# Kernel optimization log

Hardware: AMD Instinct MI355X
Metric: run time of the kernel (lower is better)

The kernel has to match this reference:

```python
import jax, jax.numpy as jnp
import numpy as np

VOCAB, D_MODEL, N_STATE, H_HEADS, LAYERS = 64, 512, 32, 16, 4
EXPAND = 2
D_INNER = EXPAND * D_MODEL          # 1024
P_HEAD = D_INNER // H_HEADS         # 64
CONV_DIM = D_INNER + 2 * N_STATE    # x, B, C share the depthwise conv
K_CONV = 4
D_IN_PROJ = 2 * D_INNER + 2 * N_STATE + H_HEADS  # z, x, B, C, dt
BATCH, SEQ = 4, 1024
EPS = 1e-5


def rmsnorm(x, w):
    return x * jax.lax.rsqrt(jnp.mean(x * x, axis=-1, keepdims=True) + EPS) * w


def silu(x):
    return x * jax.nn.sigmoid(x)


def causal_depthwise_conv(x, w, b):
    # x: [B,L,C], w: [C,K], b: [C]; causal (left) padding, depthwise groups
    xt = jnp.transpose(x, (0, 2, 1))  # [B,C,L]
    out = jax.lax.conv_general_dilated(xt, w[:, None, :], (1,), [(K_CONV - 1, 0)], feature_group_count=w.shape[0])
    return jnp.transpose(out, (0, 2, 1)) + b


def ssd(xh, dt, A, Bm, Cm, Dp):
    # Mamba2 SSD recurrence. xh [B,L,H,P], dt [B,L,H], A [H], Bm/Cm [B,L,N], Dp [H]
    dA = jnp.exp(dt * A)              # decay per (batch, step, head)
    dtx = dt[..., None] * xh          # [B,L,H,P]

    def step(h, inp):
        dA_t, dtx_t, B_t, C_t = inp
        # h: [B,H,P,N]
        h = dA_t[:, :, None, None] * h + dtx_t[..., None] * B_t[:, None, None, :]
        y = jnp.einsum('bhpn,bn->bhp', h, C_t)
        return h, y

    h0 = jnp.zeros((xh.shape[0], H_HEADS, P_HEAD, N_STATE), xh.dtype)
    _, ys = jax.lax.scan(step, h0, (jnp.moveaxis(dA, 1, 0), jnp.moveaxis(dtx, 1, 0), jnp.moveaxis(Bm, 1, 0), jnp.moveaxis(Cm, 1, 0)))
    return jnp.moveaxis(ys, 0, 1) + xh * Dp[None, None, :, None]


def mamba_block(x, norm_w, W_in, b_in, conv_w, conv_b, dt_bias, A_log, Dp, gnorm_w, W_out, b_out):
    res = x
    u = rmsnorm(x, norm_w)
    zxbcdt = u @ W_in + b_in                                # [B,L,D_IN_PROJ]
    z = zxbcdt[..., :D_INNER]
    xBC = zxbcdt[..., D_INNER:D_INNER + CONV_DIM]
    dt = zxbcdt[..., D_INNER + CONV_DIM:]                   # [B,L,H]
    xBC = silu(causal_depthwise_conv(xBC, conv_w, conv_b))
    xc = xBC[..., :D_INNER]
    Bm = xBC[..., D_INNER:D_INNER + N_STATE]
    Cm = xBC[..., D_INNER + N_STATE:]
    dt = jax.nn.softplus(dt + dt_bias)
    xh = xc.reshape(xc.shape[0], xc.shape[1], H_HEADS, P_HEAD)
    y = ssd(xh, dt, -jnp.exp(A_log), Bm, Cm, Dp)
    y = y.reshape(y.shape[0], y.shape[1], D_INNER)
    y = rmsnorm(y * silu(z), gnorm_w)                       # gated RMSNorm
    return res + y @ W_out + b_out


def forward(input_tokens, emb, norm_w, W_in, b_in, conv_w, conv_b, dt_bias, A_log, D_param, gnorm_w, W_out, b_out, head_w, head_b):
    h = emb[input_tokens]
    for i in range(LAYERS):
        h = mamba_block(h, norm_w[i], W_in[i], b_in[i], conv_w[i], conv_b[i], dt_bias[i], A_log[i], D_param[i], gnorm_w[i], W_out[i], b_out[i])
    return h @ head_w + head_b


def setup_inputs() -> dict:
    key = jax.random.key(0)
    ks = jax.random.split(key, 8)
    s = 0.02
    return {
        'input_tokens': jax.random.randint(ks[0], (BATCH, SEQ), 0, VOCAB),
        'emb': jax.random.normal(ks[1], (VOCAB, D_MODEL), jnp.float32) * s,
        'norm_w': jnp.ones((LAYERS, D_MODEL), jnp.float32),
        'W_in': jax.random.normal(ks[2], (LAYERS, D_MODEL, D_IN_PROJ), jnp.float32) * s,
        'b_in': jnp.zeros((LAYERS, D_IN_PROJ), jnp.float32),
        'conv_w': jax.random.normal(ks[3], (LAYERS, CONV_DIM, K_CONV), jnp.float32) * 0.1,
        'conv_b': jnp.zeros((LAYERS, CONV_DIM), jnp.float32),
        'dt_bias': jnp.tile(jnp.log(jnp.expm1(jnp.linspace(0.001, 0.1, H_HEADS, dtype=jnp.float32))), (LAYERS, 1)),
        'A_log': jnp.tile(jnp.log(jnp.arange(1, H_HEADS + 1, dtype=jnp.float32)), (LAYERS, 1)),
        'D_param': jnp.ones((LAYERS, H_HEADS), jnp.float32),
        'gnorm_w': jnp.ones((LAYERS, D_INNER), jnp.float32),
        'W_out': jax.random.normal(ks[4], (LAYERS, D_INNER, D_MODEL), jnp.float32) * s,
        'b_out': jnp.zeros((LAYERS, D_MODEL), jnp.float32),
        'head_w': jax.random.normal(ks[5], (D_MODEL, VOCAB), jnp.float32) * s,
        'head_b': jnp.zeros((VOCAB,), jnp.float32),
    }


def reference(input_tokens, emb, norm_w, W_in, b_in, conv_w, conv_b, dt_bias, A_log, D_param, gnorm_w, W_out, b_out, head_w, head_b):
    return forward(input_tokens, emb, norm_w, W_in, b_in, conv_w, conv_b, dt_bias, A_log, D_param, gnorm_w, W_out, b_out, head_w, head_b)
```

## Files before the change

### kernel.cpp

```cpp
#include <hip/hip_runtime.h>
#include <hip/hip_bf16.h>

#define VOCAB     64
#define D_MODEL   512
#define N_STATE   32
#define H_HEADS   16
#define LAYERS    4
#define D_INNER   1024
#define P_HEAD    64
#define CONV_DIM  1088
#define K_CONV    4
#define D_IN_PROJ 2128
#define NPAD_IN   2176
#define NPAD_HEAD 64
#define BATCH     4
#define SEQ       1024
#define NTOK      (BATCH*SEQ)
#define EPS       1e-5f
#define CL        64
#define NC        (SEQ/CL)
#define PSTR      80

typedef __bf16 bf16x8 __attribute__((ext_vector_type(8)));
typedef float  f32x4  __attribute__((ext_vector_type(4)));

__device__ __forceinline__ float sigmoidf_(float x) { return 1.f / (1.f + __expf(-x)); }
__device__ __forceinline__ float softplusf_(float x) { return (x > 20.f) ? x : log1pf(__expf(x)); }

__device__ __forceinline__ void gload_lds16(const void* g, void* l) {
  __builtin_amdgcn_global_load_lds((const __attribute__((address_space(1))) void*)g,
                                   (__attribute__((address_space(3))) void*)l,
                                   16, 0, 0);
}

__device__ __forceinline__ int xcd_lin() {
  return (blockIdx.x & 7) * ((int)gridDim.x >> 3) + ((int)blockIdx.x >> 3);
}

__global__ __launch_bounds__(256) void embed_kernel(
    const int* __restrict__ tok, const float* __restrict__ emb,
    float* __restrict__ h, __bf16* __restrict__ hbf) {
  int wv = threadIdx.x >> 6, lane = threadIdx.x & 63;
  int tokid = blockIdx.x * 4 + wv;
  const float* er = emb + (size_t)tok[tokid] * D_MODEL;
  f32x4 v0 = *(const f32x4*)(er + lane * 8);
  f32x4 v1 = *(const f32x4*)(er + lane * 8 + 4);
  float* hr = h + (size_t)tokid * D_MODEL;
  *(f32x4*)(hr + lane * 8) = v0;
  *(f32x4*)(hr + lane * 8 + 4) = v1;
  bf16x8 o8;
  #pragma unroll
  for (int k = 0; k < 4; k++) { o8[k] = (__bf16)v0[k]; o8[4 + k] = (__bf16)v1[k]; }
  *(bf16x8*)(hbf + (size_t)tokid * D_MODEL + lane * 8) = o8;
}

__global__ __launch_bounds__(256) void transpose_all_kernel(
    const float* __restrict__ W_in, const float* __restrict__ W_out,
    const float* __restrict__ head_w,
    const float* __restrict__ norm_w, const float* __restrict__ gnorm_w,
    __bf16* __restrict__ WtIn, __bf16* __restrict__ WtOut, __bf16* __restrict__ WtHead) {
  int b = blockIdx.x;
  const float* W; const float* fold; __bf16* Wt; int K, N, Npad, bx, by;
  if (b < 4352) {
    int z = b / 1088, r = b % 1088;
    bx = r % 68; by = r / 68;
    W = W_in + (size_t)z * D_MODEL * D_IN_PROJ;
    fold = norm_w + (size_t)z * D_MODEL;
    Wt = WtIn + (size_t)z * NPAD_IN * D_MODEL;
    K = D_MODEL; N = D_IN_PROJ; Npad = NPAD_IN;
  } else if (b < 6400) {
    int r = b - 4352; int z = r / 512; r %= 512;
    bx = r % 16; by = r / 16;
    W = W_out + (size_t)z * D_INNER * D_MODEL;
    fold = gnorm_w + (size_t)z * D_INNER;
    Wt = WtOut + (size_t)z * D_MODEL * D_INNER;
    K = D_INNER; N = D_MODEL; Npad = D_MODEL;
  } else {
    int r = b - 6400;
    bx = r % 2; by = r / 2;
    W = head_w; fold = nullptr; Wt = WtHead;
    K = D_MODEL; N = VOCAB; Npad = NPAD_HEAD;
  }
  __shared__ float T[32][33];
  int n0 = bx * 32, k0 = by * 32;
  int tx = threadIdx.x & 31, ty = threadIdx.x >> 5;
  #pragma unroll
  for (int i = 0; i < 4; i++) {
    int n = n0 + tx;
    T[ty + i * 8][tx] = (n < N) ? W[(size_t)(k0 + ty + i * 8) * N + n] : 0.f;
  }
  __syncthreads();
  float fs = fold ? fold[k0 + tx] : 1.f;
  #pragma unroll
  for (int i = 0; i < 4; i++)
    Wt[(size_t)(n0 + ty + i * 8) * K + k0 + tx] = (__bf16)(T[tx][ty + i * 8] * fs);
}

#define TK 64
__global__ __launch_bounds__(256) void gemm64_kernel(
    const __bf16* __restrict__ A, const __bf16* __restrict__ Bt,
    const float* __restrict__ bias, const float* __restrict__ res,
    float* __restrict__ C, __bf16* __restrict__ Cbf,
    float inv_norm_dim, int nbx, int K, int N, int ldc) {
  __shared__ __bf16 As[2][64 * TK];
  __shared__ __bf16 Bs[2][64 * TK];
  int tid = threadIdx.x;
  int lane = tid & 63, wave = tid >> 6;
  int wm = wave >> 1, wn = wave & 1;
  int q = lane >> 4, l16 = lane & 15;
  int lin = xcd_lin();
  int bx = lin % nbx, by = lin / nbx;
  size_t row0 = (size_t)by * 64;
  int col0 = bx * 64;
  const __bf16* Ab = A + row0 * K;
  const __bf16* Bb = Bt + (size_t)col0 * K;

  auto stage = [&](int buf, int kk) {
    #pragma unroll
    for (int r = 0; r < 2; r++) {
      int lin2 = r * 256 + tid;
      size_t goff = (size_t)(lin2 >> 3) * K + kk + (lin2 & 7) * 8;
      gload_lds16(Ab + goff, &As[buf][lin2 * 8]);
      gload_lds16(Bb + goff, &Bs[buf][lin2 * 8]);
    }
  };

  f32x4 acc[2][2];
  #pragma unroll
  for (int i = 0; i < 2; i++)
    #pragma unroll
    for (int j = 0; j < 2; j++) acc[i][j] = (f32x4){0.f, 0.f, 0.f, 0.f};
  float ssqa[2] = {0.f, 0.f};

  stage(0, 0);
  int cur = 0;
  for (int k0 = 0; k0 < K; k0 += TK) {
    if (k0 + TK < K) {
      stage(cur ^ 1, k0 + TK);
      asm volatile("s_waitcnt vmcnt(4)" ::: "memory");
    } else {
      asm volatile("s_waitcnt vmcnt(0)" ::: "memory");
    }
    __builtin_amdgcn_s_barrier();
    #pragma unroll
    for (int ks = 0; ks < 2; ks++) {
      bf16x8 af[2], bfv[2];
      #pragma unroll
      for (int i = 0; i < 2; i++) {
        af[i] = *(const bf16x8*)(&As[cur][(wm * 32 + i * 16 + l16) * TK + ks * 32 + q * 8]);
        #pragma unroll
        for (int k = 0; k < 8; k++) { float v = (float)af[i][k]; ssqa[i] += v * v; }
      }
      #pragma unroll
      for (int j = 0; j < 2; j++)
        bfv[j] = *(const bf16x8*)(&Bs[cur][(wn * 32 + j * 16 + l16) * TK + ks * 32 + q * 8]);
      #pragma unroll
      for (int i = 0; i < 2; i++)
        #pragma unroll
        for (int j = 0; j < 2; j++)
          acc[i][j] = __builtin_amdgcn_mfma_f32_16x16x32_bf16(af[i], bfv[j], acc[i][j], 0, 0, 0);
    }
    __builtin_amdgcn_s_barrier();
    cur ^= 1;
  }

  #pragma unroll
  for (int i = 0; i < 2; i++) {
    ssqa[i] += __shfl_xor(ssqa[i], 16);
    ssqa[i] += __shfl_xor(ssqa[i], 32);
  }
  #pragma unroll
  for (int i = 0; i < 2; i++) {
    #pragma unroll
    for (int rr = 0; rr < 4; rr++) {
      size_t mrow = row0 + wm * 32 + i * 16 + q * 4 + rr;
      float sq = __shfl(ssqa[i], q * 4 + rr);
      float sc = (inv_norm_dim > 0.f) ? rsqrtf(sq * inv_norm_dim + EPS) : 1.f;
      #pragma unroll
      for (int j = 0; j < 2; j++) {
        int col = col0 + wn * 32 + j * 16 + l16;
        if (col < N) {
          size_t off = mrow * (size_t)ldc + col;
          float v = acc[i][j][rr] * sc + (bias ? bias[col] : 0.f);
          if (res) v += res[off];
          if (C)   C[off] = v;
          if (Cbf) Cbf[off] = (__bf16)v;
        }
      }
    }
  }
}

__global__ __launch_bounds__(256) void gemm_in_kernel(
    const __bf16* __restrict__ A, const __bf16* __restrict__ Bt,
    const float* __restrict__ bias, __bf16* __restrict__ Cbf,
    int nbx, int K, int N, int ldc) {
  __shared__ __bf16 As[2][64 * TK];
  __shared__ __bf16 Bs[2][128 * TK];
  int tid = threadIdx.x;
  int lane = tid & 63, wave = tid >> 6;
  int wm = wave >> 1, wn = wave & 1;
  int q = lane >> 4, l16 = lane & 15;
  int lin = xcd_lin();
  int bx = lin % nbx, by = lin / nbx;
  size_t row0 = (size_t)by * 64;
  int col0 = bx * 128;
  const __bf16* Ab = A + row0 * K;
  const __bf16* Bb = Bt + (size_t)col0 * K;

  auto stage = [&](int buf, int kk) {
    #pragma unroll
    for (int r = 0; r < 2; r++) {
      int lin2 = r * 256 + tid;
      gload_lds16(Ab + (size_t)(lin2 >> 3) * K + kk + (lin2 & 7) * 8, &As[buf][lin2 * 8]);
    }
    #pragma unroll
    for (int r = 0; r < 4; r++) {
      int lin2 = r * 256 + tid;
      gload_lds16(Bb + (size_t)(lin2 >> 3) * K + kk + (lin2 & 7) * 8, &Bs[buf][lin2 * 8]);
    }
  };

  f32x4 acc[2][4];
  #pragma unroll
  for (int i = 0; i < 2; i++)
    #pragma unroll
    for (int j = 0; j < 4; j++) acc[i][j] = (f32x4){0.f, 0.f, 0.f, 0.f};
  float ssqa[2] = {0.f, 0.f};

  stage(0, 0);
  int cur = 0;
  for (int k0 = 0; k0 < K; k0 += TK) {
    if (k0 + TK < K) {
      stage(cur ^ 1, k0 + TK);
      asm volatile("s_waitcnt vmcnt(6)" ::: "memory");
    } else {
      asm volatile("s_waitcnt vmcnt(0)" ::: "memory");
    }
    __builtin_amdgcn_s_barrier();
    #pragma unroll
    for (int ks = 0; ks < 2; ks++) {
      bf16x8 af[2], bfv[4];
      #pragma unroll
      for (int i = 0; i < 2; i++) {
        af[i] = *(const bf16x8*)(&As[cur][(wm * 32 + i * 16 + l16) * TK + ks * 32 + q * 8]);
        #pragma unroll
        for (int k = 0; k < 8; k++) { float v = (float)af[i][k]; ssqa[i] += v * v; }
      }
      #pragma unroll
      for (int j = 0; j < 4; j++)
        bfv[j] = *(const bf16x8*)(&Bs[cur][(wn * 64 + j * 16 + l16) * TK + ks * 32 + q * 8]);
      #pragma unroll
      for (int i = 0; i < 2; i++)
        #pragma unroll
        for (int j = 0; j < 4; j++)
          acc[i][j] = __builtin_amdgcn_mfma_f32_16x16x32_bf16(af[i], bfv[j], acc[i][j], 0, 0, 0);
    }
    __builtin_amdgcn_s_barrier();
    cur ^= 1;
  }

  #pragma unroll
  for (int i = 0; i < 2; i++) {
    ssqa[i] += __shfl_xor(ssqa[i], 16);
    ssqa[i] += __shfl_xor(ssqa[i], 32);
  }
  __bf16* Cs = (__bf16*)Bs;
  const int CST = 136;
  float bvj[4];
  #pragma unroll
  for (int j = 0; j < 4; j++) {
    int colj = col0 + wn * 64 + j * 16 + l16;
    bvj[j] = (colj < N) ? bias[colj] : 0.f;
  }
  #pragma unroll
  for (int i = 0; i < 2; i++) {
    #pragma unroll
    for (int rr = 0; rr < 4; rr++) {
      int rloc = wm * 32 + i * 16 + q * 4 + rr;
      float sq = __shfl(ssqa[i], q * 4 + rr);
      float sc = rsqrtf(sq * (1.f / D_MODEL) + EPS);
      #pragma unroll
      for (int j = 0; j < 4; j++)
        Cs[rloc * CST + wn * 64 + j * 16 + l16] = (__bf16)(acc[i][j][rr] * sc + bvj[j]);
    }
  }
  __syncthreads();
  #pragma unroll
  for (int s = 0; s < 2; s++) {
    int idx = s * 256 + tid;
    int row = idx >> 3, c0 = (idx & 7) * 16;
    if (col0 + c0 < N) {
      bf16x8 v0 = *(const bf16x8*)(&Cs[row * CST + c0]);
      bf16x8 v1 = *(const bf16x8*)(&Cs[row * CST + c0 + 8]);
      __bf16* dst = Cbf + (row0 + row) * (size_t)ldc + col0 + c0;
      *(bf16x8*)dst = v0;
      *(bf16x8*)(dst + 8) = v1;
    }
  }
}

__device__ __forceinline__ void wave0_dt_cumsum(
    const __bf16* __restrict__ zxbf, const float* __restrict__ dt_bias,
    int b, int h, int t0, int tid, float* ldt, float* lcs, float* __restrict__ dtcsg) {
  if (tid < 64) {
    float dv = (float)zxbf[((size_t)(b * SEQ + t0 + tid)) * D_IN_PROJ + 2 * D_INNER + 2 * N_STATE + h]
               + dt_bias[h];
    float dtv = softplusf_(dv);
    float cs = dtv;
    #pragma unroll
    for (int off = 1; off < 64; off <<= 1) {
      float o = __shfl_up(cs, off);
      if (tid >= off) cs += o;
    }
    ldt[tid] = dtv;
    lcs[tid] = cs;
    dtcsg[tid] = dtv;
    dtcsg[64 + tid] = cs;
  }
}

__global__ __launch_bounds__(256) void ssd_local_kernel(
    const __bf16* __restrict__ zxbf, const float* __restrict__ conv_w,
    const float* __restrict__ conv_b, const float* __restrict__ dt_bias,
    const float* __restrict__ A_log,
    float* __restrict__ Slocal, float* __restrict__ dAprod,
    __bf16* __restrict__ convx, __bf16* __restrict__ convbc, float* __restrict__ dtcs) {
  int blk = xcd_lin();
  int c = blk % NC;
  int h = (blk / NC) % H_HEADS;
  int b = blk / (NC * H_HEADS);
  int tid = threadIdx.x;
  int lane = tid & 63, wave = tid >> 6;
  int q = lane >> 4, l16 = lane & 15;
  int t0 = c * CL;
  float A = -__expf(A_log[h]);
  __shared__ __bf16 rawbuf[2 * 68 * 64];
  __shared__ __bf16 lxT[64][PSTR];
  __shared__ __bf16 lBTw[32][PSTR];
  __shared__ float ldt[64], lcs[64];
  __bf16* rawx = rawbuf;
  __bf16* rawBC = rawbuf + 68 * 64;
  for (int i = tid; i < 68 * 8; i += 256) {
    int r = i >> 3, c0 = (i & 7) * 8;
    int gr = t0 - 3 + r;
    bf16x8 vx, vbc;
    #pragma unroll
    for (int k = 0; k < 8; k++) { vx[k] = (__bf16)0.f; vbc[k] = (__bf16)0.f; }
    if (gr >= 0) {
      const __bf16* rowp = zxbf + ((size_t)(b * SEQ + gr)) * D_IN_PROJ;
      vx  = *(const bf16x8*)(rowp + D_INNER + h * 64 + c0);
      vbc = *(const bf16x8*)(rowp + 2 * D_INNER + c0);
    }
    *(bf16x8*)(rawx + r * 64 + c0)  = vx;
    *(bf16x8*)(rawBC + r * 64 + c0) = vbc;
  }
  wave0_dt_cumsum(zxbf, dt_bias, b, h, t0, tid, ldt, lcs, dtcs + (size_t)blk * 128);
  __syncthreads();
  float cs63 = lcs[63];
  __bf16* xg  = convx  + (size_t)blk * 4096;
  __bf16* bcg = convbc + (size_t)blk * 4096;
  {
    int p = tid & 63;
    const float* w = conv_w + (h * 64 + p) * K_CONV;
    float w0 = w[0], w1 = w[1], w2 = w[2], w3 = w[3];
    float cb = conv_b[h * 64 + p];
    for (int i = tid; i < CL * 64; i += 256) {
      int t = i >> 6;
      float a = cb + w0 * (float)rawx[t * 64 + p] + w1 * (float)rawx[(t + 1) * 64 + p]
                   + w2 * (float)rawx[(t + 2) * 64 + p] + w3 * (float)rawx[(t + 3) * 64 + p];
      lxT[p][t] = (__bf16)(a * sigmoidf_(a));
    }
  }
  {
    int col = tid & 63;
    const float* w = conv_w + (D_INNER + col) * K_CONV;
    float w0 = w[0], w1 = w[1], w2 = w[2], w3 = w[3];
    float cb = conv_b[D_INNER + col];
    for (int i = tid; i < CL * 64; i += 256) {
      int t = i >> 6;
      float a = cb + w0 * (float)rawBC[t * 64 + col] + w1 * (float)rawBC[(t + 1) * 64 + col]
                   + w2 * (float)rawBC[(t + 2) * 64 + col] + w3 * (float)rawBC[(t + 3) * 64 + col];
      float v = a * sigmoidf_(a);
      if (col < 32) {
        bcg[t * 32 + col] = (__bf16)v;
        float wt = ldt[t] * __expf(A * (cs63 - lcs[t]));
        lBTw[col][t] = (__bf16)(v * wt);
      } else {
        bcg[2048 + t * 32 + (col - 32)] = (__bf16)v;
      }
    }
  }
  __syncthreads();
  #pragma unroll
  for (int s = 0; s < 2; s++) {
    int idx = s * 256 + tid;
    int row = idx >> 3, c0 = (idx & 7) * 8;
    *(bf16x8*)(xg + row * 64 + c0) = *(const bf16x8*)(&lxT[row][c0]);
  }
  f32x4 acc0 = (f32x4){0.f,0.f,0.f,0.f}, acc1 = (f32x4){0.f,0.f,0.f,0.f};
  #pragma unroll
  for (int kb = 0; kb < 2; kb++) {
    bf16x8 af = *(const bf16x8*)(&lxT[wave * 16 + l16][kb * 32 + q * 8]);
    bf16x8 b0 = *(const bf16x8*)(&lBTw[l16][kb * 32 + q * 8]);
    bf16x8 b1 = *(const bf16x8*)(&lBTw[l16 + 16][kb * 32 + q * 8]);
    acc0 = __builtin_amdgcn_mfma_f32_16x16x32_bf16(af, b0, acc0, 0, 0, 0);
    acc1 = __builtin_amdgcn_mfma_f32_16x16x32_bf16(af, b1, acc1, 0, 0, 0);
  }
  float* sT = (float*)rawbuf;
  #pragma unroll
  for (int rr = 0; rr < 4; rr++) {
    int p = wave * 16 + q * 4 + rr;
    sT[p * 36 + l16]      = acc0[rr];
    sT[p * 36 + l16 + 16] = acc1[rr];
  }
  {
    int row = tid >> 2, c0 = (tid & 3) * 8;
    f32x4 a = *(const f32x4*)(sT + row * 36 + c0);
    f32x4 b2 = *(const f32x4*)(sT + row * 36 + c0 + 4);
    float* dstp = Slocal + (size_t)blk * 2048 + row * 32 + c0;
    *(f32x4*)dstp = a;
    *(f32x4*)(dstp + 4) = b2;
  }
  if (tid == 0) dAprod[blk] = __expf(A * cs63);
}

__global__ __launch_bounds__(256) void ssd_out_kernel(
    const __bf16* __restrict__ zxbf, const float* __restrict__ A_log,
    const float* __restrict__ Dp,
    const float* __restrict__ Slocal, const float* __restrict__ dAprod,
    const __bf16* __restrict__ convx, const __bf16* __restrict__ convbc,
    const float* __restrict__ dtcs, __bf16* __restrict__ gout) {
  int blk = xcd_lin();
  int c = blk % NC;
  int h = (blk / NC) % H_HEADS;
  int b = blk / (NC * H_HEADS);
  int tid = threadIdx.x;
  int lane = tid & 63, wave = tid >> 6;
  int q = lane >> 4, l16 = lane & 15;
  int t0 = c * CL;
  float A = -__expf(A_log[h]);
  float D = Dp[h];
  __shared__ __bf16 lxT[64][PSTR];
  __shared__ __bf16 pPbuf[64 * PSTR];
  __shared__ __bf16 lB[64][32];
  __shared__ __bf16 lC[64][32];
  __shared__ __bf16 lS[64][32];
  __shared__ float ldt[64], lcs[64];
  __shared__ float pr[NC];
  const __bf16* xg  = convx  + (size_t)blk * 4096;
  const __bf16* bcg = convbc + (size_t)blk * 4096;
  #pragma unroll
  for (int s = 0; s < 2; s++) {
    int idx = s * 256 + tid;
    int row = idx >> 3, c0 = (idx & 7) * 8;
    *(bf16x8*)(&lxT[row][c0]) = *(const bf16x8*)(xg + row * 64 + c0);
  }
  {
    int row = tid >> 2, c0 = (tid & 3) * 8;
    *(bf16x8*)(&lB[row][c0]) = *(const bf16x8*)(bcg + row * 32 + c0);
    *(bf16x8*)(&lC[row][c0]) = *(const bf16x8*)(bcg + 2048 + row * 32 + c0);
  }
  if (tid < 64) {
    const float* dg = dtcs + (size_t)blk * 128;
    ldt[tid] = dg[tid];
    lcs[tid] = dg[64 + tid];
  }
  if (tid < NC) pr[tid] = dAprod[(blk - c) + tid];
  __syncthreads();
  {
    int p = tid >> 2, n0 = (tid & 3) * 8;
    const float* sl = Slocal + (size_t)(blk - c) * 2048 + p * 32 + n0;
    float st[8] = {};
    for (int j = 0; j < c; j++) {
      f32x4 a = *(const f32x4*)(sl + (size_t)j * 2048);
      f32x4 bq = *(const f32x4*)(sl + (size_t)j * 2048 + 4);
      float prj = pr[j];
      #pragma unroll
      for (int k = 0; k < 4; k++) { st[k] = prj * st[k] + a[k]; st[4 + k] = prj * st[4 + k] + bq[k]; }
    }
    #pragma unroll
    for (int k = 0; k < 8; k++) lS[p][n0 + k] = (__bf16)st[k];
  }
  __syncthreads();
  bf16x8 afC = *(const bf16x8*)(&lC[wave * 16 + l16][q * 8]);
  f32x4 accG[4], accI[4], accY[4];
  #pragma unroll
  for (int j = 0; j < 4; j++) {
    accG[j] = (f32x4){0.f,0.f,0.f,0.f};
    accI[j] = (f32x4){0.f,0.f,0.f,0.f};
    accY[j] = (f32x4){0.f,0.f,0.f,0.f};
  }
  #pragma unroll
  for (int j = 0; j < 4; j++) {
    bf16x8 bf = *(const bf16x8*)(&lB[l16 + 16 * j][q * 8]);
    accG[j] = __builtin_amdgcn_mfma_f32_16x16x32_bf16(afC, bf, accG[j], 0, 0, 0);
  }
  #pragma unroll
  for (int j = 0; j < 4; j++) {
    bf16x8 bf = *(const bf16x8*)(&lS[l16 + 16 * j][q * 8]);
    accI[j] = __builtin_amdgcn_mfma_f32_16x16x32_bf16(afC, bf, accI[j], 0, 0, 0);
  }
  __bf16* pP = pPbuf + wave * 16 * PSTR;
  #pragma unroll
  for (int j = 0; j < 4; j++) {
    int s = l16 + 16 * j;
    float css = lcs[s], dts = ldt[s];
    #pragma unroll
    for (int rr = 0; rr < 4; rr++) {
      int tl = q * 4 + rr;
      int t = wave * 16 + tl;
      float val = accG[j][rr] * __expf(A * (lcs[t] - css)) * dts;
      if (s == t) val += D;
      if (s > t) val = 0.f;
      pP[tl * PSTR + s] = (__bf16)val;
    }
  }
  #pragma unroll
  for (int kb = 0; kb < 2; kb++) {
    bf16x8 afP = *(const bf16x8*)(pP + l16 * PSTR + kb * 32 + q * 8);
    #pragma unroll
    for (int j = 0; j < 4; j++) {
      bf16x8 bf = *(const bf16x8*)(&lxT[l16 + 16 * j][kb * 32 + q * 8]);
      accY[j] = __builtin_amdgcn_mfma_f32_16x16x32_bf16(afP, bf, accY[j], 0, 0, 0);
    }
  }
  __syncthreads();
  __bf16* yT = pPbuf;
  #pragma unroll
  for (int rr = 0; rr < 4; rr++) {
    int t = wave * 16 + q * 4 + rr;
    float cumt = __expf(A * lcs[t]);
    #pragma unroll
    for (int j = 0; j < 4; j++) {
      int p = l16 + 16 * j;
      yT[t * 72 + p] = (__bf16)(accY[j][rr] + cumt * accI[j][rr]);
    }
  }
  {
    int row = tid >> 2, col0 = (tid & 3) * 16;
    bf16x8 y0 = *(const bf16x8*)(yT + row * 72 + col0);
    bf16x8 y1 = *(const bf16x8*)(yT + row * 72 + col0 + 8);
    const __bf16* zrow = zxbf + ((size_t)(b * SEQ + t0 + row)) * D_IN_PROJ + h * 64 + col0;
    bf16x8 z0 = *(const bf16x8*)zrow;
    bf16x8 z1 = *(const bf16x8*)(zrow + 8);
    bf16x8 g0, g1;
    #pragma unroll
    for (int k = 0; k < 8; k++) {
      float zz = (float)z0[k];
      g0[k] = (__bf16)((float)y0[k] * zz * sigmoidf_(zz));
    }
    #pragma unroll
    for (int k = 0; k < 8; k++) {
      float zz = (float)z1[k];
      g1[k] = (__bf16)((float)y1[k] * zz * sigmoidf_(zz));
    }
    __bf16* grow = gout + ((size_t)(b * SEQ + t0 + row)) * D_INNER + h * 64 + col0;
    *(bf16x8*)grow = g0;
    *(bf16x8*)(grow + 8) = g1;
  }
}

extern "C" void kernel_launch(void* const* d_in, const int* in_sizes, int n_in,
                              void* d_out, int out_size, void* d_ws, size_t ws_size,
                              hipStream_t stream) {
  const int*   tok     = (const int*)  d_in[0];
  const float* emb     = (const float*)d_in[1];
  const float* norm_w  = (const float*)d_in[2];
  const float* W_in    = (const float*)d_in[3];
  const float* b_in    = (const float*)d_in[4];
  const float* conv_w  = (const float*)d_in[5];
  const float* conv_b  = (const float*)d_in[6];
  const float* dt_bias = (const float*)d_in[7];
  const float* A_log   = (const float*)d_in[8];
  const float* D_par   = (const float*)d_in[9];
  const float* gnorm_w = (const float*)d_in[10];
  const float* W_out   = (const float*)d_in[11];
  const float* b_out   = (const float*)d_in[12];
  const float* head_w  = (const float*)d_in[13];
  const float* head_b  = (const float*)d_in[14];
  float* out = (float*)d_out;

  char* p = (char*)d_ws;
  auto alloc = [&](size_t bytes) { void* r = (void*)p; p += (bytes + 255) & ~(size_t)255; return r; };
  float*  h      = (float*) alloc((size_t)NTOK * D_MODEL * 4);
  float*  slocal = (float*) alloc((size_t)BATCH * H_HEADS * NC * P_HEAD * N_STATE * 4);
  float*  daprod = (float*) alloc((size_t)BATCH * H_HEADS * NC * 4);
  float*  dtcs   = (float*) alloc((size_t)1024 * 128 * 4);
  __bf16* convx  = (__bf16*)alloc((size_t)1024 * 4096 * 2);
  __bf16* convbc = (__bf16*)alloc((size_t)1024 * 4096 * 2);
  __bf16* zxbf   = (__bf16*)alloc((size_t)NTOK * D_IN_PROJ * 2);
  __bf16* gbf    = (__bf16*)alloc((size_t)NTOK * D_INNER * 2);
  __bf16* hbf    = (__bf16*)alloc((size_t)NTOK * D_MODEL * 2);
  __bf16* WtIn   = (__bf16*)alloc((size_t)LAYERS * NPAD_IN * D_MODEL * 2);
  __bf16* WtOut  = (__bf16*)alloc((size_t)LAYERS * D_MODEL * D_INNER * 2);
  __bf16* WtHead = (__bf16*)alloc((size_t)NPAD_HEAD * D_MODEL * 2);

  transpose_all_kernel<<<6432, 256, 0, stream>>>(
      W_in, W_out, head_w, norm_w, gnorm_w, WtIn, WtOut, WtHead);

  embed_kernel<<<NTOK / 4, 256, 0, stream>>>(tok, emb, h, hbf);

  for (int l = 0; l < LAYERS; l++) {
    gemm_in_kernel<<<1088, 256, 0, stream>>>(
        hbf, WtIn + (size_t)l * NPAD_IN * D_MODEL, b_in + (size_t)l * D_IN_PROJ,
        zxbf, NPAD_IN / 128, D_MODEL, D_IN_PROJ, D_IN_PROJ);

    ssd_local_kernel<<<BATCH * H_HEADS * NC, 256, 0, stream>>>(
        zxbf, conv_w + (size_t)l * CONV_DIM * K_CONV, conv_b + (size_t)l * CONV_DIM,
        dt_bias + (size_t)l * H_HEADS, A_log + (size_t)l * H_HEADS, slocal, daprod,
        convx, convbc, dtcs);
    ssd_out_kernel<<<BATCH * H_HEADS * NC, 256, 0, stream>>>(
        zxbf, A_log + (size_t)l * H_HEADS, D_par + (size_t)l * H_HEADS,
        slocal, daprod, convx, convbc, dtcs, gbf);

    gemm64_kernel<<<512, 256, 0, stream>>>(
        gbf, WtOut + (size_t)l * D_MODEL * D_INNER, b_out + (size_t)l * D_MODEL, h,
        h, hbf, 1.f / D_INNER, D_MODEL / 64, D_INNER, D_MODEL, D_MODEL);
  }

  gemm64_kernel<<<64, 256, 0, stream>>>(
      hbf, WtHead, head_b, nullptr, out, nullptr, 0.f, 1, D_MODEL, VOCAB, VOCAB);
}
```

Before: 444.3 us.

## Fuse embed into prep kernel, single-buffer A tile, and stream padded conv-x via LDS DMA

Merges the embedding gather into the weight-transpose kernel, which saves one launch. In gemm_in, the A tile drops to a single LDS buffer that is reloaded after the barrier, while B stays double-buffered. This lowers LDS use but exposes the A load latency. The SSD local kernel now writes the padded lxT layout directly, and ssd_out loads x/B/C straight into LDS with global_load_lds, dropping one __syncthreads. The ssd_out change has no explicit vmcnt wait before the later barrier, which may risk a correctness race.

```diff
diff --git a/kernel.cpp b/kernel.cpp
--- a/kernel.cpp
+++ b/kernel.cpp
@@ -37,29 +37,30 @@
   return (blockIdx.x & 7) * ((int)gridDim.x >> 3) + ((int)blockIdx.x >> 3);
 }
 
-__global__ __launch_bounds__(256) void embed_kernel(
-    const int* __restrict__ tok, const float* __restrict__ emb,
-    float* __restrict__ h, __bf16* __restrict__ hbf) {
-  int wv = threadIdx.x >> 6, lane = threadIdx.x & 63;
-  int tokid = blockIdx.x * 4 + wv;
-  const float* er = emb + (size_t)tok[tokid] * D_MODEL;
-  f32x4 v0 = *(const f32x4*)(er + lane * 8);
-  f32x4 v1 = *(const f32x4*)(er + lane * 8 + 4);
-  float* hr = h + (size_t)tokid * D_MODEL;
-  *(f32x4*)(hr + lane * 8) = v0;
-  *(f32x4*)(hr + lane * 8 + 4) = v1;
-  bf16x8 o8;
-  #pragma unroll
-  for (int k = 0; k < 4; k++) { o8[k] = (__bf16)v0[k]; o8[4 + k] = (__bf16)v1[k]; }
-  *(bf16x8*)(hbf + (size_t)tokid * D_MODEL + lane * 8) = o8;
-}
-
-__global__ __launch_bounds__(256) void transpose_all_kernel(
+__global__ __launch_bounds__(256) void prep_kernel(
     const float* __restrict__ W_in, const float* __restrict__ W_out,
     const float* __restrict__ head_w,
     const float* __restrict__ norm_w, const float* __restrict__ gnorm_w,
-    __bf16* __restrict__ WtIn, __bf16* __restrict__ WtOut, __bf16* __restrict__ WtHead) {
+    __bf16* __restrict__ WtIn, __bf16* __restrict__ WtOut, __bf16* __restrict__ WtHead,
+    const int* __restrict__ tok, const float* __restrict__ emb,
+    float* __restrict__ h, __bf16* __restrict__ hbf) {
   int b = blockIdx.x;
+  if (b >= 6432) {
+    int eb = b - 6432;
+    int wv = threadIdx.x >> 6, lane = threadIdx.x & 63;
+    int tokid = eb * 4 + wv;
+    const float* er = emb + (size_t)tok[tokid] * D_MODEL;
+    f32x4 v0 = *(const f32x4*)(er + lane * 8);
+    f32x4 v1 = *(const f32x4*)(er + lane * 8 + 4);
+    float* hr = h + (size_t)tokid * D_MODEL;
+    *(f32x4*)(hr + lane * 8) = v0;
+    *(f32x4*)(hr + lane * 8 + 4) = v1;
+    bf16x8 o8;
+    #pragma unroll
+    for (int k = 0; k < 4; k++) { o8[k] = (__bf16)v0[k]; o8[4 + k] = (__bf16)v1[k]; }
+    *(bf16x8*)(hbf + (size_t)tokid * D_MODEL + lane * 8) = o8;
+    return;
+  }
   const float* W; const float* fold; __bf16* Wt; int K, N, Npad, bx, by;
   if (b < 4352) {
     int z = b / 1088, r = b % 1088;
@@ -195,7 +196,7 @@
     const __bf16* __restrict__ A, const __bf16* __restrict__ Bt,
     const float* __restrict__ bias, __bf16* __restrict__ Cbf,
     int nbx, int K, int N, int ldc) {
-  __shared__ __bf16 As[2][64 * TK];
+  __shared__ __bf16 As[64 * TK];
   __shared__ __bf16 Bs[2][128 * TK];
   int tid = threadIdx.x;
   int lane = tid & 63, wave = tid >> 6;
@@ -208,12 +209,14 @@
   const __bf16* Ab = A + row0 * K;
   const __bf16* Bb = Bt + (size_t)col0 * K;
 
-  auto stage = [&](int buf, int kk) {
+  auto stageA = [&](int kk) {
     #pragma unroll
     for (int r = 0; r < 2; r++) {
       int lin2 = r * 256 + tid;
-      gload_lds16(Ab + (size_t)(lin2 >> 3) * K + kk + (lin2 & 7) * 8, &As[buf][lin2 * 8]);
-    }
+      gload_lds16(Ab + (size_t)(lin2 >> 3) * K + kk + (lin2 & 7) * 8, As + lin2 * 8);
+    }
+  };
+  auto stageB = [&](int buf, int kk) {
     #pragma unroll
     for (int r = 0; r < 4; r++) {
       int lin2 = r * 256 + tid;
@@ -228,12 +231,13 @@
     for (int j = 0; j < 4; j++) acc[i][j] = (f32x4){0.f, 0.f, 0.f, 0.f};
   float ssqa[2] = {0.f, 0.f};
 
-  stage(0, 0);
+  stageA(0);
+  stageB(0, 0);
   int cur = 0;
   for (int k0 = 0; k0 < K; k0 += TK) {
     if (k0 + TK < K) {
-      stage(cur ^ 1, k0 + TK);
-      asm volatile("s_waitcnt vmcnt(6)" ::: "memory");
+      stageB(cur ^ 1, k0 + TK);
+      asm volatile("s_waitcnt vmcnt(4)" ::: "memory");
     } else {
       asm volatile("s_waitcnt vmcnt(0)" ::: "memory");
     }
@@ -243,7 +247,7 @@
       bf16x8 af[2], bfv[4];
       #pragma unroll
       for (int i = 0; i < 2; i++) {
-        af[i] = *(const bf16x8*)(&As[cur][(wm * 32 + i * 16 + l16) * TK + ks * 32 + q * 8]);
+        af[i] = *(const bf16x8*)(&As[(wm * 32 + i * 16 + l16) * TK + ks * 32 + q * 8]);
         #pragma unroll
         for (int k = 0; k < 8; k++) { float v = (float)af[i][k]; ssqa[i] += v * v; }
       }
@@ -257,6 +261,7 @@
           acc[i][j] = __builtin_amdgcn_mfma_f32_16x16x32_bf16(af[i], bfv[j], acc[i][j], 0, 0, 0);
     }
     __builtin_amdgcn_s_barrier();
+    if (k0 + TK < K) stageA(k0 + TK);
     cur ^= 1;
   }
 
@@ -358,7 +363,7 @@
   wave0_dt_cumsum(zxbf, dt_bias, b, h, t0, tid, ldt, lcs, dtcs + (size_t)blk * 128);
   __syncthreads();
   float cs63 = lcs[63];
-  __bf16* xg  = convx  + (size_t)blk * 4096;
+  __bf16* xg  = convx  + (size_t)blk * (64 * PSTR);
   __bf16* bcg = convbc + (size_t)blk * 4096;
   {
     int p = tid & 63;
@@ -392,12 +397,8 @@
     }
   }
   __syncthreads();
-  #pragma unroll
-  for (int s = 0; s < 2; s++) {
-    int idx = s * 256 + tid;
-    int row = idx >> 3, c0 = (idx & 7) * 8;
-    *(bf16x8*)(xg + row * 64 + c0) = *(const bf16x8*)(&lxT[row][c0]);
-  }
+  for (int i = tid; i < (64 * PSTR) / 8; i += 256)
+    *(bf16x8*)(xg + i * 8) = *(const bf16x8*)(((const __bf16*)lxT) + i * 8);
   f32x4 acc0 = (f32x4){0.f,0.f,0.f,0.f}, acc1 = (f32x4){0.f,0.f,0.f,0.f};
   #pragma unroll
   for (int kb = 0; kb < 2; kb++) {
@@ -443,31 +444,24 @@
   float D = Dp[h];
   __shared__ __bf16 lxT[64][PSTR];
   __shared__ __bf16 pPbuf[64 * PSTR];
-  __shared__ __bf16 lB[64][32];
-  __shared__ __bf16 lC[64][32];
+  __shared__ __bf16 lBC[2 * 64 * 32];
   __shared__ __bf16 lS[64][32];
   __shared__ float ldt[64], lcs[64];
   __shared__ float pr[NC];
-  const __bf16* xg  = convx  + (size_t)blk * 4096;
+  const __bf16* xg  = convx  + (size_t)blk * (64 * PSTR);
   const __bf16* bcg = convbc + (size_t)blk * 4096;
-  #pragma unroll
-  for (int s = 0; s < 2; s++) {
-    int idx = s * 256 + tid;
-    int row = idx >> 3, c0 = (idx & 7) * 8;
-    *(bf16x8*)(&lxT[row][c0]) = *(const bf16x8*)(xg + row * 64 + c0);
-  }
-  {
-    int row = tid >> 2, c0 = (tid & 3) * 8;
-    *(bf16x8*)(&lB[row][c0]) = *(const bf16x8*)(bcg + row * 32 + c0);
-    *(bf16x8*)(&lC[row][c0]) = *(const bf16x8*)(bcg + 2048 + row * 32 + c0);
-  }
+  __bf16* lB = lBC;
+  __bf16* lC = lBC + 2048;
+  for (int i = tid; i < (64 * PSTR) / 8; i += 256)
+    gload_lds16(xg + i * 8, ((__bf16*)lxT) + i * 8);
+  for (int i = tid; i < 512; i += 256)
+    gload_lds16(bcg + i * 8, lBC + i * 8);
   if (tid < 64) {
     const float* dg = dtcs + (size_t)blk * 128;
     ldt[tid] = dg[tid];
     lcs[tid] = dg[64 + tid];
   }
   if (tid < NC) pr[tid] = dAprod[(blk - c) + tid];
-  __syncthreads();
   {
     int p = tid >> 2, n0 = (tid & 3) * 8;
     const float* sl = Slocal + (size_t)(blk - c) * 2048 + p * 32 + n0;
@@ -483,7 +477,7 @@
     for (int k = 0; k < 8; k++) lS[p][n0 + k] = (__bf16)st[k];
   }
   __syncthreads();
-  bf16x8 afC = *(const bf16x8*)(&lC[wave * 16 + l16][q * 8]);
+  bf16x8 afC = *(const bf16x8*)(lC + (wave * 16 + l16) * 32 + q * 8);
   f32x4 accG[4], accI[4], accY[4];
   #pragma unroll
   for (int j = 0; j < 4; j++) {
@@ -493,7 +487,7 @@
   }
   #pragma unroll
   for (int j = 0; j < 4; j++) {
-    bf16x8 bf = *(const bf16x8*)(&lB[l16 + 16 * j][q * 8]);
+    bf16x8 bf = *(const bf16x8*)(lB + (l16 + 16 * j) * 32 + q * 8);
     accG[j] = __builtin_amdgcn_mfma_f32_16x16x32_bf16(afC, bf, accG[j], 0, 0, 0);
   }
   #pragma unroll
@@ -587,7 +581,7 @@
   float*  slocal = (float*) alloc((size_t)BATCH * H_HEADS * NC * P_HEAD * N_STATE * 4);
   float*  daprod = (float*) alloc((size_t)BATCH * H_HEADS * NC * 4);
   float*  dtcs   = (float*) alloc((size_t)1024 * 128 * 4);
-  __bf16* convx  = (__bf16*)alloc((size_t)1024 * 4096 * 2);
+  __bf16* convx  = (__bf16*)alloc((size_t)1024 * 64 * PSTR * 2);
   __bf16* convbc = (__bf16*)alloc((size_t)1024 * 4096 * 2);
   __bf16* zxbf   = (__bf16*)alloc((size_t)NTOK * D_IN_PROJ * 2);
   __bf16* gbf    = (__bf16*)alloc((size_t)NTOK * D_INNER * 2);
@@ -596,10 +590,9 @@
   __bf16* WtOut  = (__bf16*)alloc((size_t)LAYERS * D_MODEL * D_INNER * 2);
   __bf16* WtHead = (__bf16*)alloc((size_t)NPAD_HEAD * D_MODEL * 2);
 
-  transpose_all_kernel<<<6432, 256, 0, stream>>>(
-      W_in, W_out, head_w, norm_w, gnorm_w, WtIn, WtOut, WtHead);
-
-  embed_kernel<<<NTOK / 4, 256, 0, stream>>>(tok, emb, h, hbf);
+  prep_kernel<<<6432 + NTOK / 4, 256, 0, stream>>>(
+      W_in, W_out, head_w, norm_w, gnorm_w, WtIn, WtOut, WtHead,
+      tok, emb, h, hbf);
 
   for (int l = 0; l < LAYERS; l++) {
     gemm_in_kernel<<<1088, 256, 0, stream>>>(
```

Result: no change. 444.3 us (-0.0%).
